# Optimization experiments

Measured on AMD Instinct MI355X. Metric: run time of the kernel, lower is better.

Reference implementation:

```python
import jax, jax.numpy as jnp
import numpy as np

N_HEAD = 16

def setup_inputs() -> dict:
    key = jax.random.key(0)
    k1, k2, k3 = jax.random.split(key, 3)
    B, T, C = 2, 2048, 1024
    x_norm_for_qk = jax.random.normal(k1, (B, T, C), dtype=jnp.float32)
    xt_current_for_v = jax.random.normal(k2, (B, T, C), dtype=jnp.float32)
    W_attn = jax.random.normal(k3, (C, 2 * C), dtype=jnp.float32) * (1.0 / np.sqrt(C))
    b_attn = jnp.zeros((2 * C,), dtype=jnp.float32)
    return {"x_norm_for_qk": x_norm_for_qk, "xt_current_for_v": xt_current_for_v,
            "W_attn": W_attn, "b_attn": b_attn}

def reference(x_norm_for_qk, xt_current_for_v, W_attn, b_attn):
    B, T, C = x_norm_for_qk.shape
    H = N_HEAD
    D = C // H  # head dim
    qk = x_norm_for_qk @ W_attn + b_attn          # [B,T,2C]
    q, k = qk[..., :C], qk[..., C:]
    q = q.reshape(B, T, H, D).transpose(0, 2, 1, 3)   # [B,H,T,D]
    k = k.reshape(B, T, H, D).transpose(0, 2, 1, 3)
    v = xt_current_for_v.reshape(B, T, H, D).transpose(0, 2, 1, 3)
    scale = 1.0 / np.sqrt(D).astype(np.float32)
    scores = jnp.einsum('bhqd,bhkd->bhqk', q, k) * scale  # [B,H,T,T]
    causal = jnp.tril(jnp.ones((T, T), dtype=bool))
    scores = jnp.where(causal[None, None], scores, jnp.float32(-jnp.inf))
    weights = jax.nn.softmax(scores, axis=-1)  # dropout p=0.0 -> identity
    y = jnp.einsum('bhqk,bhkd->bhqd', weights, v)
    return y.transpose(0, 2, 1, 3).reshape(B, T, C)
```

## Files before the change

kernel.cpp:

```cpp
#include <hip/hip_runtime.h>
#include <hip/hip_bf16.h>
#include <math.h>

typedef __attribute__((ext_vector_type(8))) short s8v;
typedef __attribute__((ext_vector_type(4))) float f4v;
typedef __attribute__((ext_vector_type(16))) float f16v;
typedef unsigned short ush;
typedef unsigned int u32;

#define QSCALE 0.180336880f

static __device__ __forceinline__ ush f2bf(float f) {
    u32 x = __builtin_bit_cast(u32, f);
    return (ush)((x + 0x7fffu + ((x >> 16) & 1u)) >> 16);
}
static __device__ __forceinline__ u32 bfpack(float lo, float hi) {
    u32 a = __builtin_bit_cast(u32, lo) + 0x8000u;
    u32 b = __builtin_bit_cast(u32, hi) + 0x8000u;
    return __builtin_amdgcn_perm(b, a, 0x07060302);
}
static __device__ __forceinline__ void gl_lds16(const void* g, void* l) {
    __builtin_amdgcn_global_load_lds(
        (const __attribute__((address_space(1))) u32*)g,
        (__attribute__((address_space(3))) u32*)l, 16, 0, 0);
}
#if __has_builtin(__builtin_amdgcn_exp2f)
#define EXP2F(x) __builtin_amdgcn_exp2f(x)
#else
#define EXP2F(x) exp2f(x)
#endif

__global__ __launch_bounds__(256) void prepA_kernel(
    const float* __restrict__ X, const float* __restrict__ W,
    ush* __restrict__ Xb, ush* __restrict__ Wt)
{
    __shared__ float Ts[64][68];
    const int tid = threadIdx.x;
    const int bid = blockIdx.x;
    if (bid < 2048) {
        const size_t i = ((size_t)bid * 256 + tid) * 8;
        float4 v0 = *(const float4*)(X + i);
        float4 v1 = *(const float4*)(X + i + 4);
        uint4 o;
        o.x = bfpack(v0.x, v0.y); o.y = bfpack(v0.z, v0.w);
        o.z = bfpack(v1.x, v1.y); o.w = bfpack(v1.z, v1.w);
        *(uint4*)(Xb + i) = o;
    } else {
        const int id = bid - 2048;
        const int n0 = (id & 31) * 64, k0 = (id >> 5) * 64;
        #pragma unroll
        for (int p = 0; p < 4; ++p) {
            const int idx = p * 256 + tid;
            const int kr = idx >> 4, nc4 = idx & 15;
            float4 v = *(const float4*)(W + (size_t)(k0 + kr) * 2048 + n0 + nc4 * 4);
            Ts[kr][nc4 * 4 + 0] = v.x; Ts[kr][nc4 * 4 + 1] = v.y;
            Ts[kr][nc4 * 4 + 2] = v.z; Ts[kr][nc4 * 4 + 3] = v.w;
        }
        __syncthreads();
        const int n = tid >> 2, kb = (tid & 3) * 16;
        #pragma unroll
        for (int p = 0; p < 4; ++p) {
            const int k = kb + p * 4;
            ushort4 o;
            o.x = f2bf(Ts[k + 0][n]); o.y = f2bf(Ts[k + 1][n]);
            o.z = f2bf(Ts[k + 2][n]); o.w = f2bf(Ts[k + 3][n]);
            *(ushort4*)(Wt + (size_t)(n0 + n) * 1024 + k0 + k) = o;
        }
    }
}

__global__ __launch_bounds__(256) void vt_kernel(
    const float* __restrict__ XV, ush* __restrict__ Vt)
{
    __shared__ float Ts[64][68];
    const int tid = threadIdx.x;
    const int t0 = blockIdx.x * 64;
    const int bh = blockIdx.y;
    const int b = bh >> 4, h = bh & 15;
    #pragma unroll
    for (int p = 0; p < 4; ++p) {
        const int idx = p * 256 + tid;
        const int tr = idx >> 4, dc4 = idx & 15;
        float4 v = *(const float4*)(XV + (size_t)(b * 2048 + t0 + tr) * 1024
                                    + h * 64 + dc4 * 4);
        Ts[tr][dc4 * 4 + 0] = v.x; Ts[tr][dc4 * 4 + 1] = v.y;
        Ts[tr][dc4 * 4 + 2] = v.z; Ts[tr][dc4 * 4 + 3] = v.w;
    }
    __syncthreads();
    const int d = tid >> 2, tb = (tid & 3) * 16;
    #pragma unroll
    for (int p = 0; p < 4; ++p) {
        const int tq = tb + p * 4;
        ushort4 o;
        o.x = f2bf(Ts[tq + 0][d]); o.y = f2bf(Ts[tq + 1][d]);
        o.z = f2bf(Ts[tq + 2][d]); o.w = f2bf(Ts[tq + 3][d]);
        *(ushort4*)(Vt + (size_t)((b * 16 + h) * 64 + d) * 2048 + t0 + tq) = o;
    }
}

__global__ __launch_bounds__(256) void gemm_kernel(
    const ush* __restrict__ Xb, const ush* __restrict__ Wt,
    const float* __restrict__ bias,
    ush* __restrict__ Qb, ush* __restrict__ Kb)
{
    __shared__ ush As[128 * 32];
    __shared__ ush Bs[128 * 32];

    const int tid = threadIdx.x;
    const int wid = tid >> 6, lane = tid & 63;
    const int quad = lane >> 4, l15 = lane & 15;
    const int wm = wid >> 1, wn = wid & 1;
    const int m0 = blockIdx.y * 128, n0 = blockIdx.x * 128;

    const int lrow = lane >> 2;
    const int lkk = (lane & 3) * 8;
    const size_t arow = (size_t)(m0 + wid * 32 + lrow);
    const size_t brow = (size_t)(n0 + wid * 32 + lrow);
    ush* AsW = &As[wid * 1024];
    ush* BsW = &Bs[wid * 1024];

    f4v acc[4][4];
    #pragma unroll
    for (int i = 0; i < 4; ++i)
        #pragma unroll
        for (int j = 0; j < 4; ++j) acc[i][j] = (f4v){0.f, 0.f, 0.f, 0.f};

    for (int k0 = 0; k0 < 1024; k0 += 32) {
        gl_lds16(Xb + arow * 1024 + k0 + lkk, AsW);
        gl_lds16(Xb + (arow + 16) * 1024 + k0 + lkk, AsW + 512);
        gl_lds16(Wt + brow * 1024 + k0 + lkk, BsW);
        gl_lds16(Wt + (brow + 16) * 1024 + k0 + lkk, BsW + 512);
        __syncthreads();

        s8v a[4], bf[4];
        #pragma unroll
        for (int i = 0; i < 4; ++i)
            a[i] = *(const s8v*)&As[(wm * 64 + i * 16 + l15) * 32 + quad * 8];
        #pragma unroll
        for (int j = 0; j < 4; ++j)
            bf[j] = *(const s8v*)&Bs[(wn * 64 + j * 16 + l15) * 32 + quad * 8];
        #pragma unroll
        for (int i = 0; i < 4; ++i)
            #pragma unroll
            for (int j = 0; j < 4; ++j)
                acc[i][j] = __builtin_amdgcn_mfma_f32_16x16x32_bf16(
                    a[i], bf[j], acc[i][j], 0, 0, 0);
        __syncthreads();
    }

    #pragma unroll
    for (int j = 0; j < 4; ++j) {
        const int n = n0 + wn * 64 + j * 16 + l15;
        const float bv = bias[n];
        const bool is_k = n >= 1024;
        const int nn = n & 1023;
        const int h = nn >> 6, d = nn & 63;
        ush* dst = is_k ? Kb : Qb;
        #pragma unroll
        for (int i = 0; i < 4; ++i) {
            const int mrow = m0 + wm * 64 + i * 16 + quad * 4;
            #pragma unroll
            for (int r = 0; r < 4; ++r) {
                const int m = mrow + r;
                const int b = m >> 11, t = m & 2047;
                float val = acc[i][j][r] + bv;
                if (!is_k) val *= QSCALE;
                dst[(size_t)((b * 16 + h) * 2048 + t) * 64 + d] = f2bf(val);
            }
        }
    }
}

__global__ __launch_bounds__(256, 2) void attn_kernel(
    const ush* __restrict__ Qb, const ush* __restrict__ Kb,
    const ush* __restrict__ Vt, float* __restrict__ Y)
{
    __shared__ ush SMEM[25600];
    ush* Kbuf = SMEM;
    ush* Vbuf = SMEM + 8192;
    ush* Pq   = SMEM + 16384;

    const int tid = threadIdx.x;
    const int w = tid >> 6, lane = tid & 63;
    const int l31 = lane & 31, hi = lane >> 5;

    const int idx = blockIdx.x;
    const int half = idx >> 8, pair = idx & 255;
    const int qt = half ? (pair & 15) : 15 - (pair & 15);
    const int bh = (pair >> 4) + half * 16;
    const int b = bh >> 4, h = bh & 15;
    const int q0 = qt * 128;
    const int ktmax = 2 * qt + 1;

    const ush* Qg = Qb + (size_t)bh * 2048 * 64;
    const ush* Kg = Kb + (size_t)bh * 2048 * 64;
    const ush* Vg = Vt + (size_t)bh * 64 * 2048;

    ush* Pw = Pq + w * 2304;

    {
        const int r8 = lane >> 3, c8 = lane & 7;
        #pragma unroll
        for (int p = 0; p < 4; ++p) {
            const int row = p * 8 + r8;
            uint4 v = *(const uint4*)(Qg + (size_t)(q0 + w * 32 + row) * 64 + c8 * 8);
            *(uint4*)&Pw[row * 72 + c8 * 8] = v;
        }
    }
    s8v bq[4];
    #pragma unroll
    for (int s = 0; s < 4; ++s)
        bq[s] = *(const s8v*)&Pw[l31 * 72 + s * 16 + hi * 8];

    const int r8 = lane >> 3;
    const int g8 = ((lane & 7) ^ r8) * 8;
    auto stage = [&](int kt, int buf) {
        const int k0e = kt * 64;
        const ush* kg = Kg + (size_t)(k0e + w * 16 + r8) * 64 + g8;
        gl_lds16(kg, &Kbuf[buf * 4096 + (w * 16) * 64]);
        gl_lds16(kg + 8 * 64, &Kbuf[buf * 4096 + (w * 16 + 8) * 64]);
        const ush* vg = Vg + (size_t)(w * 16 + r8) * 2048 + k0e + g8;
        gl_lds16(vg, &Vbuf[buf * 4096 + (w * 16) * 64]);
        gl_lds16(vg + 8 * 2048, &Vbuf[buf * 4096 + (w * 16 + 8) * 64]);
    };

    f16v acco0 = {}, acco1 = {};
    float mr = -INFINITY, lr = 0.f;
    const int qg = q0 + w * 32 + l31;

    stage(0, 0);
    __syncthreads();

    for (int kt = 0; kt <= ktmax; ++kt) {
        const int buf = kt & 1;
        if (kt < ktmax) stage(kt + 1, buf ^ 1);

        f16v s0 = {}, s1 = {};
        #pragma unroll
        for (int s = 0; s < 4; ++s) {
            const int ch = (s << 1) + hi;
            const int row0 = l31, row1 = 32 + l31;
            s8v ak0 = *(const s8v*)&Kbuf[buf * 4096 + row0 * 64 + ((ch ^ (row0 & 7)) << 3)];
            s8v ak1 = *(const s8v*)&Kbuf[buf * 4096 + row1 * 64 + ((ch ^ (row1 & 7)) << 3)];
            s0 = __builtin_amdgcn_mfma_f32_32x32x16_bf16(ak0, bq[s], s0, 0, 0, 0);
            s1 = __builtin_amdgcn_mfma_f32_32x32x16_bf16(ak1, bq[s], s1, 0, 0, 0);
        }

        const bool needmask = (kt * 64 + 63) > (q0 + w * 32);
        float mloc = -INFINITY;
        #pragma unroll
        for (int r = 0; r < 16; ++r) {
            float v0 = s0[r], v1 = s1[r];
            if (needmask) {
                const int keyb = kt * 64 + (r & 3) + 8 * (r >> 2) + 4 * hi;
                if (keyb > qg) v0 = -INFINITY;
                if (keyb + 32 > qg) v1 = -INFINITY;
                s0[r] = v0; s1[r] = v1;
            }
            mloc = fmaxf(mloc, fmaxf(v0, v1));
        }
        mloc = fmaxf(mloc, __shfl_xor(mloc, 32));
        const float mnew = fmaxf(mr, mloc);
        const float alpha = EXP2F(mr - mnew);
        mr = mnew;

        float ps = 0.f;
        #pragma unroll
        for (int g4 = 0; g4 < 4; ++g4) {
            float e0a = EXP2F(s0[g4 * 4 + 0] - mnew), e0b = EXP2F(s0[g4 * 4 + 1] - mnew);
            float e0c = EXP2F(s0[g4 * 4 + 2] - mnew), e0d = EXP2F(s0[g4 * 4 + 3] - mnew);
            float e1a = EXP2F(s1[g4 * 4 + 0] - mnew), e1b = EXP2F(s1[g4 * 4 + 1] - mnew);
            float e1c = EXP2F(s1[g4 * 4 + 2] - mnew), e1d = EXP2F(s1[g4 * 4 + 3] - mnew);
            ps += (e0a + e0b) + (e0c + e0d) + (e1a + e1b) + (e1c + e1d);
            uint2 p0; p0.x = bfpack(e0a, e0b); p0.y = bfpack(e0c, e0d);
            uint2 p1; p1.x = bfpack(e1a, e1b); p1.y = bfpack(e1c, e1d);
            const int off = g4 * 8 + hi * 4;
            *(uint2*)&Pw[l31 * 72 + off] = p0;
            *(uint2*)&Pw[l31 * 72 + 32 + off] = p1;
        }
        ps += __shfl_xor(ps, 32);
        lr = lr * alpha + ps;

        #pragma unroll
        for (int r = 0; r < 16; ++r) { acco0[r] *= alpha; acco1[r] *= alpha; }

        #pragma unroll
        for (int s = 0; s < 4; ++s) {
            s8v pf = *(const s8v*)&Pw[l31 * 72 + s * 16 + hi * 8];
            const int ch = (s << 1) + hi;
            const int row0 = l31, row1 = 32 + l31;
            s8v av0 = *(const s8v*)&Vbuf[buf * 4096 + row0 * 64 + ((ch ^ (row0 & 7)) << 3)];
            s8v av1 = *(const s8v*)&Vbuf[buf * 4096 + row1 * 64 + ((ch ^ (row1 & 7)) << 3)];
            acco0 = __builtin_amdgcn_mfma_f32_32x32x16_bf16(av0, pf, acco0, 0, 0, 0);
            acco1 = __builtin_amdgcn_mfma_f32_32x32x16_bf16(av1, pf, acco1, 0, 0, 0);
        }

        __syncthreads();
    }

    __syncthreads();
    float* LTw = (float*)SMEM + w * (32 * 68);
    const float inv = 1.0f / lr;
    #pragma unroll
    for (int r = 0; r < 16; ++r) {
        const int d = (r & 3) + 8 * (r >> 2) + 4 * hi;
        LTw[l31 * 68 + d] = acco0[r] * inv;
        LTw[l31 * 68 + 32 + d] = acco1[r] * inv;
    }
    const int qr4 = lane >> 4, chk = lane & 15;
    #pragma unroll
    for (int p = 0; p < 8; ++p) {
        const int qrow = p * 4 + qr4;
        f4v v = *(const f4v*)&LTw[qrow * 68 + chk * 4];
        *(float4*)(Y + (size_t)(b * 2048 + q0 + w * 32 + qrow) * 1024
                   + h * 64 + chk * 4) = (float4){v[0], v[1], v[2], v[3]};
    }
}

extern "C" void kernel_launch(void* const* d_in, const int* in_sizes, int n_in,
                              void* d_out, int out_size, void* d_ws,
                              size_t ws_size, hipStream_t stream)
{
    const float* x_qk = (const float*)d_in[0];
    const float* x_v  = (const float*)d_in[1];
    const float* W    = (const float*)d_in[2];
    const float* bias = (const float*)d_in[3];
    float* out = (float*)d_out;

    unsigned char* ws = (unsigned char*)d_ws;
    ush* Xb = (ush*)(ws);
    ush* Vt = (ush*)(ws);
    ush* Wt = (ush*)(ws + (8u << 20));
    ush* Qb = (ush*)(ws + (12u << 20));
    ush* Kb = (ush*)(ws + (20u << 20));

    prepA_kernel<<<2560, 256, 0, stream>>>(x_qk, W, Xb, Wt);
    gemm_kernel<<<dim3(16, 32), 256, 0, stream>>>(Xb, Wt, bias, Qb, Kb);
    vt_kernel<<<dim3(32, 32), 256, 0, stream>>>(x_v, Vt);
    attn_kernel<<<512, 256, 0, stream>>>(Qb, Kb, Vt, out);
}
```

Before: 162.5 us.

## Fuse prep kernels, convert X inside GEMM, shrink attention tiles with register P

Merges the W transpose and V transpose into one prep launch and drops the separate X→bf16 pass: the GEMM now loads fp32 X directly, converts it to bf16 and writes it into padded LDS. The attention kernel moves to 128-thread blocks covering 64 query rows each, with 1024 blocks and interleaved causal tile ordering. It keeps P in registers, using cross-half lane shuffles to build the MFMA operand instead of an LDS round trip, and masks only the diagonal tile. This removes one launch and the Xb round trip through memory, but the GEMM now does scalar-path global loads for A and each attention block covers fewer query rows, so K/V tiles are reloaded more often.

Result: slower. 195.1 us (+20.0%).

```diff
diff --git a/kernel.cpp b/kernel.cpp
--- a/kernel.cpp
+++ b/kernel.cpp
@@ -30,24 +30,15 @@
 #define EXP2F(x) exp2f(x)
 #endif
 
-__global__ __launch_bounds__(256) void prepA_kernel(
-    const float* __restrict__ X, const float* __restrict__ W,
-    ush* __restrict__ Xb, ush* __restrict__ Wt)
+__global__ __launch_bounds__(256) void prep_kernel(
+    const float* __restrict__ W, const float* __restrict__ XV,
+    ush* __restrict__ Wt, ush* __restrict__ Vt)
 {
     __shared__ float Ts[64][68];
     const int tid = threadIdx.x;
     const int bid = blockIdx.x;
-    if (bid < 2048) {
-        const size_t i = ((size_t)bid * 256 + tid) * 8;
-        float4 v0 = *(const float4*)(X + i);
-        float4 v1 = *(const float4*)(X + i + 4);
-        uint4 o;
-        o.x = bfpack(v0.x, v0.y); o.y = bfpack(v0.z, v0.w);
-        o.z = bfpack(v1.x, v1.y); o.w = bfpack(v1.z, v1.w);
-        *(uint4*)(Xb + i) = o;
-    } else {
-        const int id = bid - 2048;
-        const int n0 = (id & 31) * 64, k0 = (id >> 5) * 64;
+    if (bid < 512) {
+        const int n0 = (bid & 31) * 64, k0 = (bid >> 5) * 64;
         #pragma unroll
         for (int p = 0; p < 4; ++p) {
             const int idx = p * 256 + tid;
@@ -66,44 +57,38 @@
             o.z = f2bf(Ts[k + 2][n]); o.w = f2bf(Ts[k + 3][n]);
             *(ushort4*)(Wt + (size_t)(n0 + n) * 1024 + k0 + k) = o;
         }
-    }
-}
-
-__global__ __launch_bounds__(256) void vt_kernel(
-    const float* __restrict__ XV, ush* __restrict__ Vt)
-{
-    __shared__ float Ts[64][68];
-    const int tid = threadIdx.x;
-    const int t0 = blockIdx.x * 64;
-    const int bh = blockIdx.y;
-    const int b = bh >> 4, h = bh & 15;
-    #pragma unroll
-    for (int p = 0; p < 4; ++p) {
-        const int idx = p * 256 + tid;
-        const int tr = idx >> 4, dc4 = idx & 15;
-        float4 v = *(const float4*)(XV + (size_t)(b * 2048 + t0 + tr) * 1024
-                                    + h * 64 + dc4 * 4);
-        Ts[tr][dc4 * 4 + 0] = v.x; Ts[tr][dc4 * 4 + 1] = v.y;
-        Ts[tr][dc4 * 4 + 2] = v.z; Ts[tr][dc4 * 4 + 3] = v.w;
-    }
-    __syncthreads();
-    const int d = tid >> 2, tb = (tid & 3) * 16;
-    #pragma unroll
-    for (int p = 0; p < 4; ++p) {
-        const int tq = tb + p * 4;
-        ushort4 o;
-        o.x = f2bf(Ts[tq + 0][d]); o.y = f2bf(Ts[tq + 1][d]);
-        o.z = f2bf(Ts[tq + 2][d]); o.w = f2bf(Ts[tq + 3][d]);
-        *(ushort4*)(Vt + (size_t)((b * 16 + h) * 64 + d) * 2048 + t0 + tq) = o;
+    } else {
+        const int id = bid - 512;
+        const int t0 = (id & 31) * 64, bh = id >> 5;
+        const int b = bh >> 4, h = bh & 15;
+        #pragma unroll
+        for (int p = 0; p < 4; ++p) {
+            const int idx = p * 256 + tid;
+            const int tr = idx >> 4, dc4 = idx & 15;
+            float4 v = *(const float4*)(XV + (size_t)(b * 2048 + t0 + tr) * 1024
+                                        + h * 64 + dc4 * 4);
+            Ts[tr][dc4 * 4 + 0] = v.x; Ts[tr][dc4 * 4 + 1] = v.y;
+            Ts[tr][dc4 * 4 + 2] = v.z; Ts[tr][dc4 * 4 + 3] = v.w;
+        }
+        __syncthreads();
+        const int d = tid >> 2, tb = (tid & 3) * 16;
+        #pragma unroll
+        for (int p = 0; p < 4; ++p) {
+            const int tq = tb + p * 4;
+            ushort4 o;
+            o.x = f2bf(Ts[tq + 0][d]); o.y = f2bf(Ts[tq + 1][d]);
+            o.z = f2bf(Ts[tq + 2][d]); o.w = f2bf(Ts[tq + 3][d]);
+            *(ushort4*)(Vt + (size_t)((b * 16 + h) * 64 + d) * 2048 + t0 + tq) = o;
+        }
     }
 }
 
 __global__ __launch_bounds__(256) void gemm_kernel(
-    const ush* __restrict__ Xb, const ush* __restrict__ Wt,
+    const float* __restrict__ X, const ush* __restrict__ Wt,
     const float* __restrict__ bias,
     ush* __restrict__ Qb, ush* __restrict__ Kb)
 {
-    __shared__ ush As[128 * 32];
+    __shared__ ush As[128 * 40];
     __shared__ ush Bs[128 * 32];
 
     const int tid = threadIdx.x;
@@ -112,11 +97,11 @@
     const int wm = wid >> 1, wn = wid & 1;
     const int m0 = blockIdx.y * 128, n0 = blockIdx.x * 128;
 
-    const int lrow = lane >> 2;
-    const int lkk = (lane & 3) * 8;
-    const size_t arow = (size_t)(m0 + wid * 32 + lrow);
-    const size_t brow = (size_t)(n0 + wid * 32 + lrow);
-    ush* AsW = &As[wid * 1024];
+    const int arow = tid >> 1;
+    const int akc = (tid & 1) * 16;
+    const int brow = lane >> 2;
+    const int bkk = (lane & 3) * 8;
+    const size_t brow_g = (size_t)(n0 + wid * 32 + brow);
     ush* BsW = &Bs[wid * 1024];
 
     f4v acc[4][4];
@@ -126,16 +111,28 @@
         for (int j = 0; j < 4; ++j) acc[i][j] = (f4v){0.f, 0.f, 0.f, 0.f};
 
     for (int k0 = 0; k0 < 1024; k0 += 32) {
-        gl_lds16(Xb + arow * 1024 + k0 + lkk, AsW);
-        gl_lds16(Xb + (arow + 16) * 1024 + k0 + lkk, AsW + 512);
-        gl_lds16(Wt + brow * 1024 + k0 + lkk, BsW);
-        gl_lds16(Wt + (brow + 16) * 1024 + k0 + lkk, BsW + 512);
+        gl_lds16(Wt + brow_g * 1024 + k0 + bkk, BsW);
+        gl_lds16(Wt + (brow_g + 16) * 1024 + k0 + bkk, BsW + 512);
+        {
+            const float* xp = X + (size_t)(m0 + arow) * 1024 + k0 + akc;
+            float4 f0 = ((const float4*)xp)[0];
+            float4 f1 = ((const float4*)xp)[1];
+            float4 f2 = ((const float4*)xp)[2];
+            float4 f3 = ((const float4*)xp)[3];
+            uint4 w0, w1;
+            w0.x = bfpack(f0.x, f0.y); w0.y = bfpack(f0.z, f0.w);
+            w0.z = bfpack(f1.x, f1.y); w0.w = bfpack(f1.z, f1.w);
+            w1.x = bfpack(f2.x, f2.y); w1.y = bfpack(f2.z, f2.w);
+            w1.z = bfpack(f3.x, f3.y); w1.w = bfpack(f3.z, f3.w);
+            *(uint4*)&As[arow * 40 + akc] = w0;
+            *(uint4*)&As[arow * 40 + akc + 8] = w1;
+        }
         __syncthreads();
 
         s8v a[4], bf[4];
         #pragma unroll
         for (int i = 0; i < 4; ++i)
-            a[i] = *(const s8v*)&As[(wm * 64 + i * 16 + l15) * 32 + quad * 8];
+            a[i] = *(const s8v*)&As[(wm * 64 + i * 16 + l15) * 40 + quad * 8];
         #pragma unroll
         for (int j = 0; j < 4; ++j)
             bf[j] = *(const s8v*)&Bs[(wn * 64 + j * 16 + l15) * 32 + quad * 8];
@@ -171,69 +168,67 @@
     }
 }
 
-__global__ __launch_bounds__(256, 2) void attn_kernel(
+__global__ __launch_bounds__(128) void attn_kernel(
     const ush* __restrict__ Qb, const ush* __restrict__ Kb,
     const ush* __restrict__ Vt, float* __restrict__ Y)
 {
-    __shared__ ush SMEM[25600];
+    __shared__ ush SMEM[16384];
     ush* Kbuf = SMEM;
     ush* Vbuf = SMEM + 8192;
-    ush* Pq   = SMEM + 16384;
 
     const int tid = threadIdx.x;
     const int w = tid >> 6, lane = tid & 63;
     const int l31 = lane & 31, hi = lane >> 5;
 
     const int idx = blockIdx.x;
-    const int half = idx >> 8, pair = idx & 255;
-    const int qt = half ? (pair & 15) : 15 - (pair & 15);
-    const int bh = (pair >> 4) + half * 16;
+    const int bh = idx >> 5, j = idx & 31;
+    const int qt = (j & 1) ? (j >> 1) : 31 - (j >> 1);
     const int b = bh >> 4, h = bh & 15;
-    const int q0 = qt * 128;
-    const int ktmax = 2 * qt + 1;
+    const int q0 = qt * 64;
 
     const ush* Qg = Qb + (size_t)bh * 2048 * 64;
     const ush* Kg = Kb + (size_t)bh * 2048 * 64;
     const ush* Vg = Vt + (size_t)bh * 64 * 2048;
-
-    ush* Pw = Pq + w * 2304;
-
-    {
-        const int r8 = lane >> 3, c8 = lane & 7;
-        #pragma unroll
-        for (int p = 0; p < 4; ++p) {
-            const int row = p * 8 + r8;
-            uint4 v = *(const uint4*)(Qg + (size_t)(q0 + w * 32 + row) * 64 + c8 * 8);
-            *(uint4*)&Pw[row * 72 + c8 * 8] = v;
-        }
-    }
-    s8v bq[4];
-    #pragma unroll
-    for (int s = 0; s < 4; ++s)
-        bq[s] = *(const s8v*)&Pw[l31 * 72 + s * 16 + hi * 8];
 
     const int r8 = lane >> 3;
     const int g8 = ((lane & 7) ^ r8) * 8;
     auto stage = [&](int kt, int buf) {
         const int k0e = kt * 64;
-        const ush* kg = Kg + (size_t)(k0e + w * 16 + r8) * 64 + g8;
-        gl_lds16(kg, &Kbuf[buf * 4096 + (w * 16) * 64]);
-        gl_lds16(kg + 8 * 64, &Kbuf[buf * 4096 + (w * 16 + 8) * 64]);
-        const ush* vg = Vg + (size_t)(w * 16 + r8) * 2048 + k0e + g8;
-        gl_lds16(vg, &Vbuf[buf * 4096 + (w * 16) * 64]);
-        gl_lds16(vg + 8 * 2048, &Vbuf[buf * 4096 + (w * 16 + 8) * 64]);
+        #pragma unroll
+        for (int i = 0; i < 4; ++i) {
+            const int rowb = w * 32 + i * 8;
+            gl_lds16(Kg + (size_t)(k0e + rowb + r8) * 64 + g8,
+                     &Kbuf[buf * 4096 + rowb * 64]);
+            gl_lds16(Vg + (size_t)(rowb + r8) * 2048 + k0e + g8,
+                     &Vbuf[buf * 4096 + rowb * 64]);
+        }
     };
+
+    stage(0, 0);
+    ush* Qtmp = SMEM + 12288 + w * 2048;
+    {
+        const int c8 = lane & 7;
+        #pragma unroll
+        for (int p = 0; p < 4; ++p) {
+            const int qrow = p * 8 + r8;
+            uint4 v = *(const uint4*)(Qg + (size_t)(q0 + w * 32 + qrow) * 64 + c8 * 8);
+            *(uint4*)&Qtmp[qrow * 64 + c8 * 8] = v;
+        }
+    }
+    __syncthreads();
+    s8v bq[4];
+    #pragma unroll
+    for (int s = 0; s < 4; ++s)
+        bq[s] = *(const s8v*)&Qtmp[l31 * 64 + s * 16 + hi * 8];
+    __syncthreads();
 
     f16v acco0 = {}, acco1 = {};
     float mr = -INFINITY, lr = 0.f;
     const int qg = q0 + w * 32 + l31;
 
-    stage(0, 0);
-    __syncthreads();
-
-    for (int kt = 0; kt <= ktmax; ++kt) {
+    for (int kt = 0; kt <= qt; ++kt) {
         const int buf = kt & 1;
-        if (kt < ktmax) stage(kt + 1, buf ^ 1);
+        if (kt < qt) stage(kt + 1, buf ^ 1);
 
         f16v s0 = {}, s1 = {};
         #pragma unroll
@@ -246,18 +241,20 @@
             s1 = __builtin_amdgcn_mfma_f32_32x32x16_bf16(ak1, bq[s], s1, 0, 0, 0);
         }
 
-        const bool needmask = (kt * 64 + 63) > (q0 + w * 32);
         float mloc = -INFINITY;
-        #pragma unroll
-        for (int r = 0; r < 16; ++r) {
-            float v0 = s0[r], v1 = s1[r];
-            if (needmask) {
+        if (kt == qt) {
+            #pragma unroll
+            for (int r = 0; r < 16; ++r) {
                 const int keyb = kt * 64 + (r & 3) + 8 * (r >> 2) + 4 * hi;
-                if (keyb > qg) v0 = -INFINITY;
-                if (keyb + 32 > qg) v1 = -INFINITY;
+                float v0 = (keyb > qg) ? -INFINITY : s0[r];
+                float v1 = (keyb + 32 > qg) ? -INFINITY : s1[r];
                 s0[r] = v0; s1[r] = v1;
+                mloc = fmaxf(mloc, fmaxf(v0, v1));
             }
-            mloc = fmaxf(mloc, fmaxf(v0, v1));
+        } else {
+            #pragma unroll
+            for (int r = 0; r < 16; ++r)
+                mloc = fmaxf(mloc, fmaxf(s0[r], s1[r]));
         }
         mloc = fmaxf(mloc, __shfl_xor(mloc, 32));
         const float mnew = fmaxf(mr, mloc);
@@ -265,18 +262,13 @@
         mr = mnew;
 
         float ps = 0.f;
-        #pragma unroll
-        for (int g4 = 0; g4 < 4; ++g4) {
-            float e0a = EXP2F(s0[g4 * 4 + 0] - mnew), e0b = EXP2F(s0[g4 * 4 + 1] - mnew);
-            float e0c = EXP2F(s0[g4 * 4 + 2] - mnew), e0d = EXP2F(s0[g4 * 4 + 3] - mnew);
-            float e1a = EXP2F(s1[g4 * 4 + 0] - mnew), e1b = EXP2F(s1[g4 * 4 + 1] - mnew);
-            float e1c = EXP2F(s1[g4 * 4 + 2] - mnew), e1d = EXP2F(s1[g4 * 4 + 3] - mnew);
-            ps += (e0a + e0b) + (e0c + e0d) + (e1a + e1b) + (e1c + e1d);
-            uint2 p0; p0.x = bfpack(e0a, e0b); p0.y = bfpack(e0c, e0d);
-            uint2 p1; p1.x = bfpack(e1a, e1b); p1.y = bfpack(e1c, e1d);
-            const int off = g4 * 8 + hi * 4;
-            *(uint2*)&Pw[l31 * 72 + off] = p0;
-            *(uint2*)&Pw[l31 * 72 + 32 + off] = p1;
+        u32 P0[8], P1[8];
+        #pragma unroll
+        for (int p = 0; p < 8; ++p) {
+            float a0 = EXP2F(s0[2 * p] - mnew), b0 = EXP2F(s0[2 * p + 1] - mnew);
+            float a1 = EXP2F(s1[2 * p] - mnew), b1 = EXP2F(s1[2 * p + 1] - mnew);
+            ps += (a0 + b0) + (a1 + b1);
+            P0[p] = bfpack(a0, b0); P1[p] = bfpack(a1, b1);
         }
         ps += __shfl_xor(ps, 32);
         lr = lr * alpha + ps;
@@ -285,20 +277,33 @@
         for (int r = 0; r < 16; ++r) { acco0[r] *= alpha; acco1[r] *= alpha; }
 
         #pragma unroll
-        for (int s = 0; s < 4; ++s) {
-            s8v pf = *(const s8v*)&Pw[l31 * 72 + s * 16 + hi * 8];
-            const int ch = (s << 1) + hi;
-            const int row0 = l31, row1 = 32 + l31;
-            s8v av0 = *(const s8v*)&Vbuf[buf * 4096 + row0 * 64 + ((ch ^ (row0 & 7)) << 3)];
-            s8v av1 = *(const s8v*)&Vbuf[buf * 4096 + row1 * 64 + ((ch ^ (row1 & 7)) << 3)];
-            acco0 = __builtin_amdgcn_mfma_f32_32x32x16_bf16(av0, pf, acco0, 0, 0, 0);
-            acco1 = __builtin_amdgcn_mfma_f32_32x32x16_bf16(av1, pf, acco1, 0, 0, 0);
-        }
-
-        __syncthreads();
-    }
-
-    __syncthreads();
+        for (int t = 0; t < 2; ++t) {
+            const u32* pt = t ? P1 : P0;
+            #pragma unroll
+            for (int ss = 0; ss < 2; ++ss) {
+                const int b4 = ss * 4;
+                const u32 x0 = __shfl_xor(pt[b4 + 0], 32);
+                const u32 x1 = __shfl_xor(pt[b4 + 1], 32);
+                const u32 x2 = __shfl_xor(pt[b4 + 2], 32);
+                const u32 x3 = __shfl_xor(pt[b4 + 3], 32);
+                uint4 fr;
+                fr.x = hi ? x2 : pt[b4 + 0];
+                fr.y = hi ? x3 : pt[b4 + 1];
+                fr.z = hi ? pt[b4 + 2] : x0;
+                fr.w = hi ? pt[b4 + 3] : x1;
+                const s8v pf = __builtin_bit_cast(s8v, fr);
+                const int sg = t * 2 + ss, ch = (sg << 1) + hi;
+                const int row0 = l31, row1 = 32 + l31;
+                s8v av0 = *(const s8v*)&Vbuf[buf * 4096 + row0 * 64 + ((ch ^ (row0 & 7)) << 3)];
+                s8v av1 = *(const s8v*)&Vbuf[buf * 4096 + row1 * 64 + ((ch ^ (row1 & 7)) << 3)];
+                acco0 = __builtin_amdgcn_mfma_f32_32x32x16_bf16(av0, pf, acco0, 0, 0, 0);
+                acco1 = __builtin_amdgcn_mfma_f32_32x32x16_bf16(av1, pf, acco1, 0, 0, 0);
+            }
+        }
+
+        __syncthreads();
+    }
+
     float* LTw = (float*)SMEM + w * (32 * 68);
     const float inv = 1.0f / lr;
     #pragma unroll
@@ -307,10 +312,10 @@
         LTw[l31 * 68 + d] = acco0[r] * inv;
         LTw[l31 * 68 + 32 + d] = acco1[r] * inv;
     }
-    const int qr4 = lane >> 4, chk = lane & 15;
+    const int qr2 = lane >> 4, chk = lane & 15;
     #pragma unroll
     for (int p = 0; p < 8; ++p) {
-        const int qrow = p * 4 + qr4;
+        const int qrow = p * 4 + qr2;
         f4v v = *(const f4v*)&LTw[qrow * 68 + chk * 4];
         *(float4*)(Y + (size_t)(b * 2048 + q0 + w * 32 + qrow) * 1024
                    + h * 64 + chk * 4) = (float4){v[0], v[1], v[2], v[3]};
@@ -328,14 +333,12 @@
     float* out = (float*)d_out;
 
     unsigned char* ws = (unsigned char*)d_ws;
-    ush* Xb = (ush*)(ws);
-    ush* Vt = (ush*)(ws);
-    ush* Wt = (ush*)(ws + (8u << 20));
+    ush* Wt = (ush*)(ws);
+    ush* Vt = (ush*)(ws + (4u << 20));
     ush* Qb = (ush*)(ws + (12u << 20));
     ush* Kb = (ush*)(ws + (20u << 20));
 
-    prepA_kernel<<<2560, 256, 0, stream>>>(x_qk, W, Xb, Wt);
-    gemm_kernel<<<dim3(16, 32), 256, 0, stream>>>(Xb, Wt, bias, Qb, Kb);
-    vt_kernel<<<dim3(32, 32), 256, 0, stream>>>(x_v, Vt);
-    attn_kernel<<<512, 256, 0, stream>>>(Qb, Kb, Vt, out);
-}
+    prep_kernel<<<1536, 256, 0, stream>>>(W, x_v, Wt, Vt);
+    gemm_kernel<<<dim3(16, 32), 256, 0, stream>>>(x_qk, Wt, bias, Qb, Kb);
+    attn_kernel<<<1024, 128, 0, stream>>>(Qb, Kb, Vt, out);
+}
```
